# Optimization experiments

Measured on AMD Instinct MI355X. Metric: run time of the kernel, lower is better.

The kernel has to match this reference:

```python
import jax, jax.numpy as jnp
import numpy as np

N, L, C, KF = 32, 1024, 3, 256
H = C * KF            # hidden_dim = 768
M = 3072              # mlp_dim
EPS = 1e-6


def setup_inputs() -> dict:
    key = jax.random.key(0)
    ks = jax.random.split(key, 14)
    s = lambda fan: 1.0 / np.sqrt(fan)
    return {
        "x": jax.random.normal(ks[0], (N, L, H), dtype=jnp.float32),
        # per-channel QKV linears: Linear(k_factor, 3*k_factor) for each channel
        "W_qkv": jax.random.normal(ks[1], (C, KF, 3 * KF), dtype=jnp.float32) * s(KF),
        "b_qkv": jax.random.normal(ks[2], (C, 3 * KF), dtype=jnp.float32) * 0.01,
        "W_out": jax.random.normal(ks[3], (KF, KF), dtype=jnp.float32) * s(KF),
        "b_out": jax.random.normal(ks[4], (KF,), dtype=jnp.float32) * 0.01,
        "ln1_g": jnp.ones((H,), jnp.float32),
        "ln1_b": jnp.zeros((H,), jnp.float32),
        "ln2_g": jnp.ones((H,), jnp.float32),
        "ln2_b": jnp.zeros((H,), jnp.float32),
        "W1": jax.random.normal(ks[5], (H, M), dtype=jnp.float32) * s(H),
        "b1": jax.random.normal(ks[6], (M,), dtype=jnp.float32) * 1e-6,
        "W2": jax.random.normal(ks[7], (M, H), dtype=jnp.float32) * s(M),
        "b2": jax.random.normal(ks[8], (H,), dtype=jnp.float32) * 1e-6,
    }


def _ln(x, g, b):
    mu = jnp.mean(x, axis=-1, keepdims=True)
    var = jnp.mean(jnp.square(x - mu), axis=-1, keepdims=True)
    return (x - mu) * jax.lax.rsqrt(var + EPS) * g + b


def _criss_cross_attn(h, W_qkv, b_qkv, W_out, b_out):
    # h: [N, L, H]; hidden layout is channel-major: (C, KF)
    hc = h.reshape(h.shape[0], h.shape[1], C, KF)
    qkv = jnp.einsum("nlck,ckd->nlcd", hc, W_qkv) + b_qkv      # [N,L,C,3KF]
    q, k, v = jnp.split(qkv, 3, axis=-1)                        # each [N,L,C,KF]
    # move k_factor axis before channel axis: [N,L,KF,C]
    q = jnp.swapaxes(q, -1, -2)
    k = jnp.swapaxes(k, -1, -2)
    v = jnp.swapaxes(v, -1, -2)
    # outer-product scores over channels: [N,L,KF,C,C]
    scores = q[..., :, None] * k[..., None, :] / np.sqrt(KF)
    attn = jax.nn.softmax(scores, axis=-1)
    # einsum 'ijklm,ijkl->ijkm': sum over first channel axis
    ctx = jnp.einsum("nlkcd,nlkc->nlkd", attn, v)               # [N,L,KF,C]
    ctx = jnp.swapaxes(ctx, -1, -2)                             # [N,L,C,KF]
    out = ctx @ W_out + b_out                                   # fc_out per k_factor
    return out.reshape(h.shape[0], h.shape[1], H)


def reference(x, W_qkv, b_qkv, W_out, b_out, ln1_g, ln1_b, ln2_g, ln2_b, W1, b1, W2, b2):
    h = _ln(x, ln1_g, ln1_b)
    a = _criss_cross_attn(h, W_qkv, b_qkv, W_out, b_out)
    xr = a + x                                                   # residual (dropout=0)
    y = _ln(xr, ln2_g, ln2_b)
    y = jax.nn.gelu(y @ W1 + b1, approximate=False) @ W2 + b2    # MLPBlock
    return xr + y
```

## Files before the change

kernel.cpp:

```cpp
#include <hip/hip_runtime.h>
#include <hip/hip_bf16.h>
#include <math.h>

typedef __attribute__((ext_vector_type(8))) short short8;
typedef __attribute__((ext_vector_type(4))) float f32x4;

__device__ __forceinline__ float bf2f(__hip_bfloat16 h) { return __bfloat162float(h); }
__device__ __forceinline__ __hip_bfloat16 f2bf(float f) { return __float2bfloat16(f); }

__device__ __forceinline__ float gelu_f(float v) {
  const float u = v * (0.7978845608f + 0.0356774081f * v * v);
  const float e = __expf(2.0f * u);
  const float t = 1.0f - 2.0f * __builtin_amdgcn_rcpf(e + 1.0f);
  return 0.5f * v * (1.0f + t);
}

__global__ __launch_bounds__(192) void ln_kernel(
    const float* __restrict__ in, const float* __restrict__ g,
    const float* __restrict__ b, __hip_bfloat16* __restrict__ out)
{
  __shared__ float sm1[3], sm2[3];
  const int row = blockIdx.x;
  const int tid = threadIdx.x;
  const float4 x = *(const float4*)(in + (size_t)row * 768 + tid * 4);
  float s = x.x + x.y + x.z + x.w;
  #pragma unroll
  for (int off = 32; off > 0; off >>= 1) s += __shfl_down(s, off, 64);
  const int l = tid & 63, w = tid >> 6;
  if (l == 0) sm1[w] = s;
  __syncthreads();
  const float mu = (sm1[0] + sm1[1] + sm1[2]) * (1.0f / 768.0f);
  const float d0 = x.x - mu, d1 = x.y - mu, d2 = x.z - mu, d3 = x.w - mu;
  float ss = d0*d0 + d1*d1 + d2*d2 + d3*d3;
  #pragma unroll
  for (int off = 32; off > 0; off >>= 1) ss += __shfl_down(ss, off, 64);
  if (l == 0) sm2[w] = ss;
  __syncthreads();
  const float var = (sm2[0] + sm2[1] + sm2[2]) * (1.0f / 768.0f);
  const float rstd = rsqrtf(var + 1e-6f);
  const float4 gg = *(const float4*)(g + tid * 4);
  const float4 bb = *(const float4*)(b + tid * 4);
  __hip_bfloat162* q = (__hip_bfloat162*)(out + (size_t)row * 768);
  q[tid*2]     = __hip_bfloat162{f2bf(d0 * rstd * gg.x + bb.x), f2bf(d1 * rstd * gg.y + bb.y)};
  q[tid*2 + 1] = __hip_bfloat162{f2bf(d2 * rstd * gg.z + bb.z), f2bf(d3 * rstd * gg.w + bb.w)};
}

__global__ __launch_bounds__(256) void attn_kernel(
    const __hip_bfloat162* __restrict__ qkv, __hip_bfloat162* __restrict__ ctx)
{
  const long t = (long)blockIdx.x * 256 + threadIdx.x;
  const long row = t >> 7;
  const int kp = (int)(t & 127);
  const __hip_bfloat162* p = qkv + row * 1152;
  float q[3][2], k[3][2], v[3][2];
  #pragma unroll
  for (int c = 0; c < 3; ++c) {
    __hip_bfloat162 qq = p[c*384 + kp];
    __hip_bfloat162 kk = p[c*384 + 128 + kp];
    __hip_bfloat162 vv = p[c*384 + 256 + kp];
    q[c][0] = __low2float(qq); q[c][1] = __high2float(qq);
    k[c][0] = __low2float(kk); k[c][1] = __high2float(kk);
    v[c][0] = __low2float(vv); v[c][1] = __high2float(vv);
  }
  float o[3][2] = {};
  #pragma unroll
  for (int u = 0; u < 2; ++u) {
    #pragma unroll
    for (int c = 0; c < 3; ++c) {
      const float s0 = q[c][u]*k[0][u]*0.0625f, s1 = q[c][u]*k[1][u]*0.0625f, s2 = q[c][u]*k[2][u]*0.0625f;
      const float m = fmaxf(s0, fmaxf(s1, s2));
      const float e0 = __expf(s0-m), e1 = __expf(s1-m), e2 = __expf(s2-m);
      const float inv = v[c][u] / (e0 + e1 + e2);
      o[0][u] += e0*inv; o[1][u] += e1*inv; o[2][u] += e2*inv;
    }
  }
  __hip_bfloat162* po = ctx + row * 384;
  #pragma unroll
  for (int d = 0; d < 3; ++d)
    po[d*128 + kp] = __hip_bfloat162{f2bf(o[d][0]), f2bf(o[d][1])};
}

__global__ __launch_bounds__(256) void transpose_bf16_kernel(
    const float* __restrict__ in, __hip_bfloat16* __restrict__ out, int K, int N)
{
  __shared__ float tile[32][33];
  in  += (size_t)blockIdx.z * K * N;
  out += (size_t)blockIdx.z * K * N;
  const int n0 = blockIdx.x * 32;
  const int k0 = blockIdx.y * 32;
  const int tx = threadIdx.x & 31, ty = threadIdx.x >> 5;
  #pragma unroll
  for (int r = 0; r < 32; r += 8)
    tile[ty + r][tx] = in[(size_t)(k0 + ty + r) * N + n0 + tx];
  __syncthreads();
  #pragma unroll
  for (int r = 0; r < 32; r += 8)
    out[(size_t)(n0 + ty + r) * K + k0 + tx] = f2bf(tile[tx][ty + r]);
}

#define BM 128
#define BN 128
#define BK 32

template<int MODE>
__global__ __launch_bounds__(256) void gemm_bt_kernel(
    const __hip_bfloat16* __restrict__ A, int lda, long strideA,
    const __hip_bfloat16* __restrict__ Bt, int ldb, long strideB,
    float* __restrict__ Cf, __hip_bfloat16* __restrict__ Cb, int ldc, long strideC,
    const float* __restrict__ bias, long strideBias,
    const float* __restrict__ res,
    int K)
{
  __shared__ __align__(16) char sAll[2 * 16384];

  const int z = blockIdx.z;
  A    += (size_t)z * strideA;
  Bt   += (size_t)z * strideB;
  bias += (size_t)z * strideBias;
  const long cOff = (long)z * strideC;

  const int nwg = gridDim.x * gridDim.y;
  int wg = blockIdx.x + gridDim.x * blockIdx.y;
  if ((nwg & 7) == 0) wg = (wg & 7) * (nwg >> 3) + (wg >> 3);
  const long tileM = (long)(wg % gridDim.x) * BM;
  const int  tileN = (wg / gridDim.x) * BN;

  const int tid  = threadIdx.x;
  const int lane = tid & 63;
  const int wv   = tid >> 6;
  const int waveM = (wv & 1) * 64;
  const int waveN = (wv >> 1) * 64;

  const int srow  = tid >> 2;
  const int selem = ((tid & 3) ^ ((srow >> 1) & 3)) * 8;
  const int frow = lane & 15;
  const int fkb  = (((lane >> 4) ^ ((frow >> 1) & 3)) << 4);

  const __hip_bfloat16* Ab = A  + tileM * (size_t)lda + selem;
  const __hip_bfloat16* Bb = Bt + (long)tileN * (size_t)ldb + selem;

  f32x4 acc[4][4] = {};

  const int T = K / BK;

  {
    #pragma unroll
    for (int hh = 0; hh < 2; ++hh) {
      const int r = hh * 64 + srow;
      __builtin_amdgcn_global_load_lds(
          (const __attribute__((address_space(1))) void*)(Ab + (size_t)r * lda),
          (__attribute__((address_space(3))) void*)(sAll + hh*4096 + tid*16), 16, 0, 0);
      __builtin_amdgcn_global_load_lds(
          (const __attribute__((address_space(1))) void*)(Bb + (size_t)r * ldb),
          (__attribute__((address_space(3))) void*)(sAll + 8192 + hh*4096 + tid*16), 16, 0, 0);
    }
  }

  for (int t = 0; t < T; ++t) {
    const int buf = (t & 1) * 16384;
    if (t + 1 < T) {
      const int nbuf = 16384 - buf;
      const int k0 = (t + 1) * BK;
      #pragma unroll
      for (int hh = 0; hh < 2; ++hh) {
        const int r = hh * 64 + srow;
        __builtin_amdgcn_global_load_lds(
            (const __attribute__((address_space(1))) void*)(Ab + (size_t)r * lda + k0),
            (__attribute__((address_space(3))) void*)(sAll + nbuf + hh*4096 + tid*16), 16, 0, 0);
        __builtin_amdgcn_global_load_lds(
            (const __attribute__((address_space(1))) void*)(Bb + (size_t)r * ldb + k0),
            (__attribute__((address_space(3))) void*)(sAll + nbuf + 8192 + hh*4096 + tid*16), 16, 0, 0);
      }
      asm volatile("s_waitcnt vmcnt(4)" ::: "memory");
    } else {
      asm volatile("s_waitcnt vmcnt(0)" ::: "memory");
    }
    __builtin_amdgcn_s_barrier();
    asm volatile("" ::: "memory");

    const char* sAb = sAll + buf;
    const char* sBb = sAb + 8192;
    short8 aF[4], bF[4];
    #pragma unroll
    for (int i = 0; i < 4; ++i)
      aF[i] = *(const short8*)(sAb + (waveM + i*16 + frow) * 64 + fkb);
    #pragma unroll
    for (int j = 0; j < 4; ++j)
      bF[j] = *(const short8*)(sBb + (waveN + j*16 + frow) * 64 + fkb);
    #pragma unroll
    for (int i = 0; i < 4; ++i)
      #pragma unroll
      for (int j = 0; j < 4; ++j)
        acc[i][j] = __builtin_amdgcn_mfma_f32_16x16x32_bf16(aF[i], bF[j], acc[i][j], 0, 0, 0);

    __builtin_amdgcn_s_barrier();
  }

  #pragma unroll
  for (int i = 0; i < 4; ++i) {
    const long row0 = tileM + waveM + i*16 + ((lane >> 4) * 4);
    #pragma unroll
    for (int j = 0; j < 4; ++j) {
      const int col = tileN + waveN + j*16 + (lane & 15);
      const float bv = bias[col];
      #pragma unroll
      for (int r = 0; r < 4; ++r) {
        const long idx = cOff + (row0 + r) * (long)ldc + col;
        const float v = acc[i][j][r] + bv;
        if (MODE == 0) {
          Cb[idx] = f2bf(v);
        } else if (MODE == 1 || MODE == 3) {
          Cf[idx] = v + res[idx];
        } else {
          Cb[idx] = f2bf(gelu_f(v));
        }
      }
    }
  }
}

#define GLL16(src, dst) __builtin_amdgcn_global_load_lds( \
    (const __attribute__((address_space(1))) void*)(src), \
    (__attribute__((address_space(3))) void*)(dst), 16, 0, 0)

#define STAGE_AH(h, pb, koff) do { \
    GLL16(Ab + (size_t)((h)*128 + 0 ) * lda + (koff), sAll + (pb)*65536 + (h)*16384 + 0    + tid*16); \
    GLL16(Ab + (size_t)((h)*128 + 64) * lda + (koff), sAll + (pb)*65536 + (h)*16384 + 8192 + tid*16); \
  } while (0)
#define STAGE_BH(h, pb, koff) do { \
    GLL16(Bb + (size_t)((h)*128 + 0 ) * ldb + (koff), sAll + (pb)*65536 + 32768 + (h)*16384 + 0    + tid*16); \
    GLL16(Bb + (size_t)((h)*128 + 64) * ldb + (koff), sAll + (pb)*65536 + 32768 + (h)*16384 + 8192 + tid*16); \
  } while (0)

template<int MODE>
__global__ __launch_bounds__(512, 2) void gemm256_kernel(
    const __hip_bfloat16* __restrict__ A, int lda, long strideA,
    const __hip_bfloat16* __restrict__ Bt, int ldb, long strideB,
    float* __restrict__ Cf, __hip_bfloat16* __restrict__ Cb, int ldc, long strideC,
    const float* __restrict__ bias, long strideBias,
    const float* __restrict__ res,
    int K)
{
  __shared__ __align__(16) char sAll[2 * 65536];

  const int z = blockIdx.z;
  A    += (size_t)z * strideA;
  Bt   += (size_t)z * strideB;
  bias += (size_t)z * strideBias;
  const long cOff = (long)z * strideC;

  const int nwg = gridDim.x * gridDim.y;
  int wg = blockIdx.x + gridDim.x * blockIdx.y;
  if ((nwg & 7) == 0) wg = (wg & 7) * (nwg >> 3) + (wg >> 3);
  const long tileM = (long)(wg % gridDim.x) * 256;
  const int  tileN = (wg / gridDim.x) * 256;

  const int tid  = threadIdx.x;
  const int lane = tid & 63;
  const int wv   = tid >> 6;
  const int wm   = wv & 1;
  const int wn   = wv >> 1;

  const int srow  = tid >> 3;
  const int selem = ((tid & 7) ^ (srow & 7)) * 8;

  const __hip_bfloat16* Ab = A  + (tileM + srow) * (size_t)lda + selem;
  const __hip_bfloat16* Bb = Bt + ((long)tileN + srow) * (size_t)ldb + selem;

  const int fk   = lane >> 4;
  const int fx   = lane & 7;
  const int arow = (wm*64 + (lane & 15)) * 128;
  const int brow = (wn*32 + (lane & 15)) * 128;
  const int ax0  = ((0*4 + fk) ^ fx) * 16;
  const int ax1  = ((1*4 + fk) ^ fx) * 16;

  f32x4 acc[2][2][4][2] = {};
  const int T = K / 64;

  STAGE_AH(0, 0, 0);
  STAGE_BH(0, 0, 0);
  STAGE_BH(1, 0, 0);
  STAGE_AH(1, 0, 0);
  {
    const int k1 = (T > 1 ? 1 : 0) * 64;
    STAGE_AH(0, 1, k1);
    STAGE_BH(1, 1, k1);
  }

  for (int t = 0; t < T; ++t) {
    const int p = t & 1;
    const int q = p ^ 1;
    const int kn1 = (t + 1 < T ? t + 1 : T - 1) * 64;
    const int kn2 = (t + 2 < T ? t + 2 : T - 1) * 64;
    const char* sA = sAll + p * 65536;
    const char* sB = sA + 32768;

    short8 aF[4][2], bF0[2][2], bF1[2][2];

    asm volatile("s_waitcnt vmcnt(4)" ::: "memory");
    __builtin_amdgcn_s_barrier();
    asm volatile("" ::: "memory");
    #pragma unroll
    for (int i = 0; i < 4; ++i) {
      aF[i][0] = *(const short8*)(sA + arow + i*2048 + ax0);
      aF[i][1] = *(const short8*)(sA + arow + i*2048 + ax1);
    }
    #pragma unroll
    for (int j = 0; j < 2; ++j) {
      bF0[j][0] = *(const short8*)(sB + brow + j*2048 + ax0);
      bF0[j][1] = *(const short8*)(sB + brow + j*2048 + ax1);
    }
    STAGE_AH(1, q, kn1);
    asm volatile("s_waitcnt lgkmcnt(0)" ::: "memory");
    __builtin_amdgcn_sched_barrier(0);
    __builtin_amdgcn_s_setprio(1);
    #pragma unroll
    for (int i = 0; i < 4; ++i)
      #pragma unroll
      for (int j = 0; j < 2; ++j) {
        acc[0][0][i][j] = __builtin_amdgcn_mfma_f32_16x16x32_bf16(aF[i][0], bF0[j][0], acc[0][0][i][j], 0, 0, 0);
        acc[0][0][i][j] = __builtin_amdgcn_mfma_f32_16x16x32_bf16(aF[i][1], bF0[j][1], acc[0][0][i][j], 0, 0, 0);
      }
    __builtin_amdgcn_s_setprio(0);
    __builtin_amdgcn_s_barrier();

    #pragma unroll
    for (int j = 0; j < 2; ++j) {
      bF1[j][0] = *(const short8*)(sB + 16384 + brow + j*2048 + ax0);
      bF1[j][1] = *(const short8*)(sB + 16384 + brow + j*2048 + ax1);
    }
    STAGE_BH(0, q, kn1);
    asm volatile("s_waitcnt lgkmcnt(0)" ::: "memory");
    __builtin_amdgcn_sched_barrier(0);
    __builtin_amdgcn_s_setprio(1);
    #pragma unroll
    for (int i = 0; i < 4; ++i)
      #pragma unroll
      for (int j = 0; j < 2; ++j) {
        acc[0][1][i][j] = __builtin_amdgcn_mfma_f32_16x16x32_bf16(aF[i][0], bF1[j][0], acc[0][1][i][j], 0, 0, 0);
        acc[0][1][i][j] = __builtin_amdgcn_mfma_f32_16x16x32_bf16(aF[i][1], bF1[j][1], acc[0][1][i][j], 0, 0, 0);
      }
    __builtin_amdgcn_s_setprio(0);
    __builtin_amdgcn_s_barrier();

    #pragma unroll
    for (int i = 0; i < 4; ++i) {
      aF[i][0] = *(const short8*)(sA + 16384 + arow + i*2048 + ax0);
      aF[i][1] = *(const short8*)(sA + 16384 + arow + i*2048 + ax1);
    }
    STAGE_AH(0, p, kn2);
    asm volatile("s_waitcnt lgkmcnt(0)" ::: "memory");
    __builtin_amdgcn_sched_barrier(0);
    __builtin_amdgcn_s_setprio(1);
    #pragma unroll
    for (int i = 0; i < 4; ++i)
      #pragma unroll
      for (int j = 0; j < 2; ++j) {
        acc[1][1][i][j] = __builtin_amdgcn_mfma_f32_16x16x32_bf16(aF[i][0], bF1[j][0], acc[1][1][i][j], 0, 0, 0);
        acc[1][1][i][j] = __builtin_amdgcn_mfma_f32_16x16x32_bf16(aF[i][1], bF1[j][1], acc[1][1][i][j], 0, 0, 0);
      }
    __builtin_amdgcn_s_setprio(0);

    STAGE_BH(1, p, kn2);
    __builtin_amdgcn_s_setprio(1);
    #pragma unroll
    for (int i = 0; i < 4; ++i)
      #pragma unroll
      for (int j = 0; j < 2; ++j) {
        acc[1][0][i][j] = __builtin_amdgcn_mfma_f32_16x16x32_bf16(aF[i][0], bF0[j][0], acc[1][0][i][j], 0, 0, 0);
        acc[1][0][i][j] = __builtin_amdgcn_mfma_f32_16x16x32_bf16(aF[i][1], bF0[j][1], acc[1][0][i][j], 0, 0, 0);
      }
    __builtin_amdgcn_s_setprio(0);
  }

  asm volatile("s_waitcnt vmcnt(0)" ::: "memory");

  #pragma unroll
  for (int ih = 0; ih < 2; ++ih)
    #pragma unroll
    for (int jh = 0; jh < 2; ++jh)
      #pragma unroll
      for (int i = 0; i < 4; ++i) {
        const long row0 = tileM + ih*128 + wm*64 + i*16 + ((lane >> 4) * 4);
        #pragma unroll
        for (int j = 0; j < 2; ++j) {
          const int col = tileN + jh*128 + wn*32 + j*16 + (lane & 15);
          const float bv = bias[col];
          #pragma unroll
          for (int r = 0; r < 4; ++r) {
            const long idx = cOff + (row0 + r) * (long)ldc + col;
            const float v = acc[ih][jh][i][j][r] + bv;
            if (MODE == 0) {
              Cb[idx] = f2bf(v);
            } else if (MODE == 1 || MODE == 3) {
              Cf[idx] = v + res[idx];
            } else {
              Cb[idx] = f2bf(gelu_f(v));
            }
          }
        }
      }
}

extern "C" void kernel_launch(void* const* d_in, const int* in_sizes, int n_in,
                              void* d_out, int out_size, void* d_ws, size_t ws_size,
                              hipStream_t stream)
{
  const float* x     = (const float*)d_in[0];
  const float* W_qkv = (const float*)d_in[1];
  const float* b_qkv = (const float*)d_in[2];
  const float* W_out = (const float*)d_in[3];
  const float* b_out = (const float*)d_in[4];
  const float* ln1_g = (const float*)d_in[5];
  const float* ln1_b = (const float*)d_in[6];
  const float* ln2_g = (const float*)d_in[7];
  const float* ln2_b = (const float*)d_in[8];
  const float* W1    = (const float*)d_in[9];
  const float* b1    = (const float*)d_in[10];
  const float* W2    = (const float*)d_in[11];
  const float* b2    = (const float*)d_in[12];
  float* out = (float*)d_out;

  char* ws = (char*)d_ws;
  __hip_bfloat16* h     = (__hip_bfloat16*)(ws + 0);
  __hip_bfloat16* qkv   = (__hip_bfloat16*)(ws + 50331648);
  __hip_bfloat16* ctx   = (__hip_bfloat16*)(ws + 0);
  __hip_bfloat16* act   = (__hip_bfloat16*)(ws + 0);
  __hip_bfloat16* yln   = (__hip_bfloat16*)(ws + 201326592);
  __hip_bfloat16* wqkvT = (__hip_bfloat16*)(ws + 251658240);
  __hip_bfloat16* woutT = (__hip_bfloat16*)(ws + 252837888);
  __hip_bfloat16* w1T   = (__hip_bfloat16*)(ws + 252968960);
  __hip_bfloat16* w2T   = (__hip_bfloat16*)(ws + 257687552);

  transpose_bf16_kernel<<<dim3(768/32, 256/32, 3), 256, 0, stream>>>(W_qkv, wqkvT, 256, 768);
  transpose_bf16_kernel<<<dim3(256/32, 256/32, 1), 256, 0, stream>>>(W_out, woutT, 256, 256);
  transpose_bf16_kernel<<<dim3(3072/32, 768/32, 1), 256, 0, stream>>>(W1, w1T, 768, 3072);
  transpose_bf16_kernel<<<dim3(768/32, 3072/32, 1), 256, 0, stream>>>(W2, w2T, 3072, 768);

  ln_kernel<<<32768, 192, 0, stream>>>(x, ln1_g, ln1_b, h);

  gemm256_kernel<0><<<dim3(32768/256, 768/256, 3), 512, 0, stream>>>(
      h, 768, 256, wqkvT, 256, 768*256, nullptr, qkv, 2304, 768, b_qkv, 768, nullptr, 256);

  attn_kernel<<<16384, 256, 0, stream>>>((const __hip_bfloat162*)qkv, (__hip_bfloat162*)ctx);

  gemm_bt_kernel<1><<<dim3(98304/BM, 256/BN, 1), 256, 0, stream>>>(
      ctx, 256, 0, woutT, 256, 0, out, nullptr, 256, 0, b_out, 0, x, 256);

  ln_kernel<<<32768, 192, 0, stream>>>(out, ln2_g, ln2_b, yln);

  gemm256_kernel<2><<<dim3(32768/256, 3072/256, 1), 512, 0, stream>>>(
      yln, 768, 0, w1T, 768, 0, nullptr, act, 3072, 0, b1, 0, nullptr, 768);

  gemm256_kernel<3><<<dim3(32768/256, 768/256, 1), 512, 0, stream>>>(
      act, 3072, 0, w2T, 3072, 0, out, nullptr, 768, 0, b2, 0, out, 3072);
}
```

Before: 783.5 us.

## Rework 256-tile GEMM barrier schedule and drop workgroup swizzle

Removes the XCD-style workgroup index remapping in both GEMM kernels and uses plain blockIdx tile coordinates. In the 256x256 GEMM it moves the vmcnt wait and barrier out of the loop head into finer-grained barriers after each LDS read phase. It also adds a separate aG register set for the second A half so the last two MFMA groups do not overwrite aF, aiming to overlap global stages with compute in ping-pong fashion across the two waves per SIMD. The cost is more registers, extra barriers per iteration, and possibly worse L2 locality without the swizzle.

```diff
diff --git a/kernel.cpp b/kernel.cpp
--- a/kernel.cpp
+++ b/kernel.cpp
@@ -119,11 +119,8 @@
   bias += (size_t)z * strideBias;
   const long cOff = (long)z * strideC;
 
-  const int nwg = gridDim.x * gridDim.y;
-  int wg = blockIdx.x + gridDim.x * blockIdx.y;
-  if ((nwg & 7) == 0) wg = (wg & 7) * (nwg >> 3) + (wg >> 3);
-  const long tileM = (long)(wg % gridDim.x) * BM;
-  const int  tileN = (wg / gridDim.x) * BN;
+  const long tileM = (long)blockIdx.x * BM;
+  const int  tileN = blockIdx.y * BN;
 
   const int tid  = threadIdx.x;
   const int lane = tid & 63;
@@ -249,11 +246,8 @@
   bias += (size_t)z * strideBias;
   const long cOff = (long)z * strideC;
 
-  const int nwg = gridDim.x * gridDim.y;
-  int wg = blockIdx.x + gridDim.x * blockIdx.y;
-  if ((nwg & 7) == 0) wg = (wg & 7) * (nwg >> 3) + (wg >> 3);
-  const long tileM = (long)(wg % gridDim.x) * 256;
-  const int  tileN = (wg / gridDim.x) * 256;
+  const long tileM = (long)blockIdx.x * 256;
+  const int  tileN = blockIdx.y * 256;
 
   const int tid  = threadIdx.x;
   const int lane = tid & 63;
@@ -286,6 +280,8 @@
     STAGE_AH(0, 1, k1);
     STAGE_BH(1, 1, k1);
   }
+  asm volatile("s_waitcnt vmcnt(4)" ::: "memory");
+  __builtin_amdgcn_s_barrier();
 
   for (int t = 0; t < T; ++t) {
     const int p = t & 1;
@@ -295,11 +291,8 @@
     const char* sA = sAll + p * 65536;
     const char* sB = sA + 32768;
 
-    short8 aF[4][2], bF0[2][2], bF1[2][2];
-
-    asm volatile("s_waitcnt vmcnt(4)" ::: "memory");
-    __builtin_amdgcn_s_barrier();
-    asm volatile("" ::: "memory");
+    short8 aF[4][2], aG[4][2], bF0[2][2], bF1[2][2];
+
     #pragma unroll
     for (int i = 0; i < 4; ++i) {
       aF[i][0] = *(const short8*)(sA + arow + i*2048 + ax0);
@@ -311,6 +304,9 @@
       bF0[j][1] = *(const short8*)(sB + brow + j*2048 + ax1);
     }
     STAGE_AH(1, q, kn1);
+    asm volatile("s_waitcnt lgkmcnt(8)" ::: "memory");
+    asm volatile("" ::: "memory");
+    __builtin_amdgcn_s_barrier();
     asm volatile("s_waitcnt lgkmcnt(0)" ::: "memory");
     __builtin_amdgcn_sched_barrier(0);
     __builtin_amdgcn_s_setprio(1);
@@ -330,6 +326,8 @@
       bF1[j][1] = *(const short8*)(sB + 16384 + brow + j*2048 + ax1);
     }
     STAGE_BH(0, q, kn1);
+    asm volatile("" ::: "memory");
+    __builtin_amdgcn_s_barrier();
     asm volatile("s_waitcnt lgkmcnt(0)" ::: "memory");
     __builtin_amdgcn_sched_barrier(0);
     __builtin_amdgcn_s_setprio(1);
@@ -345,10 +343,12 @@
 
     #pragma unroll
     for (int i = 0; i < 4; ++i) {
-      aF[i][0] = *(const short8*)(sA + 16384 + arow + i*2048 + ax0);
-      aF[i][1] = *(const short8*)(sA + 16384 + arow + i*2048 + ax1);
+      aG[i][0] = *(const short8*)(sA + 16384 + arow + i*2048 + ax0);
+      aG[i][1] = *(const short8*)(sA + 16384 + arow + i*2048 + ax1);
     }
     STAGE_AH(0, p, kn2);
+    asm volatile("" ::: "memory");
+    __builtin_amdgcn_s_barrier();
     asm volatile("s_waitcnt lgkmcnt(0)" ::: "memory");
     __builtin_amdgcn_sched_barrier(0);
     __builtin_amdgcn_s_setprio(1);
@@ -356,21 +356,27 @@
     for (int i = 0; i < 4; ++i)
       #pragma unroll
       for (int j = 0; j < 2; ++j) {
-        acc[1][1][i][j] = __builtin_amdgcn_mfma_f32_16x16x32_bf16(aF[i][0], bF1[j][0], acc[1][1][i][j], 0, 0, 0);
-        acc[1][1][i][j] = __builtin_amdgcn_mfma_f32_16x16x32_bf16(aF[i][1], bF1[j][1], acc[1][1][i][j], 0, 0, 0);
+        acc[1][1][i][j] = __builtin_amdgcn_mfma_f32_16x16x32_bf16(aG[i][0], bF1[j][0], acc[1][1][i][j], 0, 0, 0);
+        acc[1][1][i][j] = __builtin_amdgcn_mfma_f32_16x16x32_bf16(aG[i][1], bF1[j][1], acc[1][1][i][j], 0, 0, 0);
       }
     __builtin_amdgcn_s_setprio(0);
+    __builtin_amdgcn_s_barrier();
 
     STAGE_BH(1, p, kn2);
+    asm volatile("s_waitcnt vmcnt(4)" ::: "memory");
+    asm volatile("" ::: "memory");
+    __builtin_amdgcn_s_barrier();
+    __builtin_amdgcn_sched_barrier(0);
     __builtin_amdgcn_s_setprio(1);
     #pragma unroll
     for (int i = 0; i < 4; ++i)
       #pragma unroll
       for (int j = 0; j < 2; ++j) {
-        acc[1][0][i][j] = __builtin_amdgcn_mfma_f32_16x16x32_bf16(aF[i][0], bF0[j][0], acc[1][0][i][j], 0, 0, 0);
-        acc[1][0][i][j] = __builtin_amdgcn_mfma_f32_16x16x32_bf16(aF[i][1], bF0[j][1], acc[1][0][i][j], 0, 0, 0);
+        acc[1][0][i][j] = __builtin_amdgcn_mfma_f32_16x16x32_bf16(aG[i][0], bF0[j][0], acc[1][0][i][j], 0, 0, 0);
+        acc[1][0][i][j] = __builtin_amdgcn_mfma_f32_16x16x32_bf16(aG[i][1], bF0[j][1], acc[1][0][i][j], 0, 0, 0);
       }
     __builtin_amdgcn_s_setprio(0);
+    __builtin_amdgcn_s_barrier();
   }
 
   asm volatile("s_waitcnt vmcnt(0)" ::: "memory");
```

New measurement: 803.6 us. 1.03x slower.
